# Kernel optimization log

Hardware: AMD Instinct MI355X
Metric: run time of the kernel (lower is better)

The kernel has to match this reference:

```python
import jax, jax.numpy as jnp
import numpy as np

M, N = 24, 12
H1 = (M + N) * 10 * 8        # 2880
HID = (M * M + N * N) * 10   # 7200
H2 = M * N * 4               # 1152
DOUT = M * N                 # 288
EPS = 1e-12


def setup_inputs() -> dict:
    key = jax.random.key(0)
    ks = jax.random.split(key, 16)
    s = 0.02  # weight scale
    return {
        "yt": jax.random.normal(ks[0], (N,), jnp.float32),
        "F": jax.random.normal(ks[1], (M, M), jnp.float32) * 0.1,
        "Hm": jax.random.normal(ks[2], (N, M), jnp.float32) * 0.1,
        "m1x_posterior": jax.random.normal(ks[3], (M, 1), jnp.float32),
        "m1x_prior_old": jax.random.normal(ks[4], (M, 1), jnp.float32),
        "hn": jax.random.normal(ks[5], (HID,), jnp.float32),
        "W1": jax.random.normal(ks[6], (H1, M + N), jnp.float32) * s,
        "b1": jax.random.normal(ks[7], (H1,), jnp.float32) * s,
        "Wih": jax.random.normal(ks[8], (3 * HID, H1), jnp.float32) * s,
        "Whh": jax.random.normal(ks[9], (3 * HID, HID), jnp.float32) * s,
        "bih": jax.random.normal(ks[10], (3 * HID,), jnp.float32) * s,
        "bhh": jax.random.normal(ks[11], (3 * HID,), jnp.float32) * s,
        "W2": jax.random.normal(ks[12], (H2, HID), jnp.float32) * s,
        "b2": jax.random.normal(ks[13], (H2,), jnp.float32) * s,
        "W3": jax.random.normal(ks[14], (DOUT, H2), jnp.float32) * s,
        "b3": jax.random.normal(ks[15], (DOUT,), jnp.float32) * s,
    }


def _l2_normalize(x):
    # torch F.normalize(p=2, dim=0, eps=1e-12)
    return x / jnp.maximum(jnp.linalg.norm(x), EPS)


def _gru_cell(x, h, Wih, Whh, bih, bhh):
    gi = Wih @ x + bih            # [3*HID]
    gh = Whh @ h + bhh            # [3*HID]
    gi_r, gi_z, gi_n = jnp.split(gi, 3)
    gh_r, gh_z, gh_n = jnp.split(gh, 3)
    r = jax.nn.sigmoid(gi_r + gh_r)
    z = jax.nn.sigmoid(gi_z + gh_z)
    n = jnp.tanh(gi_n + r * gh_n)
    return (1.0 - z) * n + z * h


def reference(yt, F, Hm, m1x_posterior, m1x_prior_old, hn,
              W1, b1, Wih, Whh, bih, bhh, W2, b2, W3, b3):
    # step_prior
    m1x_prior = F @ m1x_posterior        # [M,1]
    m1y = Hm @ m1x_prior                 # [N,1]
    # step_KGain_est
    dm1x = _l2_normalize((m1x_posterior - m1x_prior_old)[:, 0])  # [M]
    dm1y = _l2_normalize(yt - m1y[:, 0])                         # [N]
    kg_in = jnp.concatenate([dm1y, dm1x])                        # [M+N]
    l1 = jax.nn.relu(W1 @ kg_in + b1)                            # [H1]
    h_new = _gru_cell(l1, hn, Wih, Whh, bih, bhh)                # [HID]
    l2 = jax.nn.relu(W2 @ h_new + b2)                            # [H2]
    kg = (W3 @ l2 + b3).reshape(M, N)                            # Kalman gain
    # KNet_step update
    dy = yt[:, None] - m1y                                       # [N,1]
    m1x_post_new = m1x_prior + kg @ dy                           # [M,1]
    return m1x_post_new[:, 0]
```

## Files before the change

### kernel.cpp

```cpp
#include <hip/hip_runtime.h>
#include <math.h>

#define M_DIM 24
#define N_DIM 12
#define H1    2880
#define HID   7200
#define H2    1152
#define DOUT  288
#define KGIN  (M_DIM + N_DIM)

#define WS_PRIOR 0
#define WS_DY    96
#define WS_L1    128
#define WS_HNEW  3072
#define WS_L2    10304
#define WS_GI    11520

__device__ __forceinline__ float wave_sum(float v) {
    #pragma unroll
    for (int o = 32; o; o >>= 1) v += __shfl_xor(v, o);
    return v;
}

__global__ __launch_bounds__(256) void k_l1h(
        const float* __restrict__ yt, const float* __restrict__ F,
        const float* __restrict__ Hm, const float* __restrict__ post,
        const float* __restrict__ prior_old,
        const float* __restrict__ W1, const float* __restrict__ b1,
        float* __restrict__ ws) {
    __shared__ float s_prior[M_DIM];
    __shared__ float s_m1y[N_DIM];
    __shared__ float s_x[KGIN];
    __shared__ float s_dy[N_DIM];
    int t = threadIdx.x, lane = t & 63, w = t >> 6;

    if (t < M_DIM) {
        float acc = 0.f;
        #pragma unroll
        for (int j = 0; j < M_DIM; ++j) acc += F[t * M_DIM + j] * post[j];
        s_prior[t] = acc;
    }
    __syncthreads();
    if (t < N_DIM) {
        float acc = 0.f;
        #pragma unroll
        for (int j = 0; j < M_DIM; ++j) acc += Hm[t * M_DIM + j] * s_prior[j];
        s_m1y[t] = acc;
    }
    __syncthreads();
    if (w == 0) {
        float vx = 0.f;
        if (lane < M_DIM) vx = post[lane] - prior_old[lane];
        float nx = fmaxf(sqrtf(wave_sum(vx * vx)), 1e-12f);
        float vy = 0.f;
        if (lane < N_DIM) vy = yt[lane] - s_m1y[lane];
        float ny = fmaxf(sqrtf(wave_sum(vy * vy)), 1e-12f);
        if (lane < N_DIM) { s_x[lane] = vy / ny; s_dy[lane] = vy; }
        if (lane < M_DIM) s_x[N_DIM + lane] = vx / nx;
    }
    __syncthreads();

    if (blockIdx.x == 0) {
        if (t < M_DIM) ws[WS_PRIOR + t] = s_prior[t];
        if (t < N_DIM) ws[WS_DY + t] = s_dy[t];
    }

    int i = blockIdx.x * 4 + w;
    float acc = (lane < KGIN) ? W1[(size_t)i * KGIN + lane] * s_x[lane] : 0.f;
    acc = wave_sum(acc);
    if (lane == 0) ws[WS_L1 + i] = fmaxf(acc + b1[i], 0.f);
}

__global__ __launch_bounds__(256, 8) void k_gi(
        const float* __restrict__ Wih, const float* __restrict__ bih,
        float* __restrict__ ws) {
    int t = threadIdx.x, lane = t & 63, w = t >> 6;
    int i = blockIdx.x * 4 + w;
    const float4* x1 = (const float4*)(ws + WS_L1);
    const float4* wr = (const float4*)(Wih + (size_t)i * H1);
    const float4* wz = (const float4*)(Wih + (size_t)(i + HID) * H1);
    const float4* wn = (const float4*)(Wih + (size_t)(i + 2 * HID) * H1);
    float ar = 0.f, az = 0.f, an = 0.f;
    #pragma unroll 2
    for (int k = lane; k < H1 / 4; k += 64) {
        float4 x = x1[k];
        float4 a = wr[k], b = wz[k], c = wn[k];
        ar += a.x * x.x + a.y * x.y + a.z * x.z + a.w * x.w;
        az += b.x * x.x + b.y * x.y + b.z * x.z + b.w * x.w;
        an += c.x * x.x + c.y * x.y + c.z * x.z + c.w * x.w;
    }
    ar = wave_sum(ar); az = wave_sum(az); an = wave_sum(an);
    if (lane == 0) {
        ws[WS_GI + i]           = ar + bih[i];
        ws[WS_GI + HID + i]     = az + bih[i + HID];
        ws[WS_GI + 2 * HID + i] = an + bih[i + 2 * HID];
    }
}

__global__ __launch_bounds__(256, 8) void k_gh(
        const float* __restrict__ Whh, const float* __restrict__ bhh,
        const float* __restrict__ hn, float* __restrict__ ws) {
    int t = threadIdx.x, lane = t & 63, w = t >> 6;
    int i = blockIdx.x * 4 + w;
    const float4* xh = (const float4*)hn;
    const float4* ur = (const float4*)(Whh + (size_t)i * HID);
    const float4* uz = (const float4*)(Whh + (size_t)(i + HID) * HID);
    const float4* un = (const float4*)(Whh + (size_t)(i + 2 * HID) * HID);
    float hr = 0.f, hz = 0.f, hh = 0.f;
    #pragma unroll 2
    for (int k = lane; k < HID / 4; k += 64) {
        float4 x = xh[k];
        float4 a = ur[k], b = uz[k], c = un[k];
        hr += a.x * x.x + a.y * x.y + a.z * x.z + a.w * x.w;
        hz += b.x * x.x + b.y * x.y + b.z * x.z + b.w * x.w;
        hh += c.x * x.x + c.y * x.y + c.z * x.z + c.w * x.w;
    }
    hr = wave_sum(hr); hz = wave_sum(hz); hh = wave_sum(hh);
    if (lane == 0) {
        float gr = ws[WS_GI + i] + hr + bhh[i];
        float gz = ws[WS_GI + HID + i] + hz + bhh[i + HID];
        float r = 1.f / (1.f + expf(-gr));
        float z = 1.f / (1.f + expf(-gz));
        float n = tanhf(ws[WS_GI + 2 * HID + i] + r * (hh + bhh[i + 2 * HID]));
        ws[WS_HNEW + i] = (1.f - z) * n + z * hn[i];
    }
}

__global__ __launch_bounds__(256, 8) void k_l2(
        const float* __restrict__ W2, const float* __restrict__ b2,
        float* __restrict__ ws) {
    int t = threadIdx.x, lane = t & 63, w = t >> 6;
    int i = blockIdx.x * 4 + w;
    const float4* x4 = (const float4*)(ws + WS_HNEW);
    const float4* wr = (const float4*)(W2 + (size_t)i * HID);
    float acc = 0.f;
    #pragma unroll 2
    for (int k = lane; k < HID / 4; k += 64) {
        float4 x = x4[k];
        float4 a = wr[k];
        acc += a.x * x.x + a.y * x.y + a.z * x.z + a.w * x.w;
    }
    acc = wave_sum(acc);
    if (lane == 0) ws[WS_L2 + i] = fmaxf(acc + b2[i], 0.f);
}

__global__ __launch_bounds__(768) void k_kg_out(
        const float* __restrict__ W3, const float* __restrict__ b3,
        const float* __restrict__ ws, float* __restrict__ out) {
    __shared__ float s_kg[N_DIM];
    int m = blockIdx.x;
    int t = threadIdx.x, lane = t & 63, w = t >> 6;
    int row = m * N_DIM + w;
    const float4* wr = (const float4*)(W3 + (size_t)row * H2);
    const float4* x4 = (const float4*)(ws + WS_L2);
    float acc = 0.f;
    for (int k = lane; k < H2 / 4; k += 64) {
        float4 x = x4[k];
        float4 a = wr[k];
        acc += a.x * x.x + a.y * x.y + a.z * x.z + a.w * x.w;
    }
    acc = wave_sum(acc);
    if (lane == 0) s_kg[w] = acc + b3[row];
    __syncthreads();
    if (t == 0) {
        float a = ws[WS_PRIOR + m];
        #pragma unroll
        for (int n = 0; n < N_DIM; ++n) a += s_kg[n] * ws[WS_DY + n];
        out[m] = a;
    }
}

extern "C" void kernel_launch(void* const* d_in, const int* in_sizes, int n_in,
                              void* d_out, int out_size, void* d_ws, size_t ws_size,
                              hipStream_t stream) {
    const float* yt        = (const float*)d_in[0];
    const float* F         = (const float*)d_in[1];
    const float* Hm        = (const float*)d_in[2];
    const float* post      = (const float*)d_in[3];
    const float* prior_old = (const float*)d_in[4];
    const float* hn        = (const float*)d_in[5];
    const float* W1        = (const float*)d_in[6];
    const float* b1        = (const float*)d_in[7];
    const float* Wih       = (const float*)d_in[8];
    const float* Whh       = (const float*)d_in[9];
    const float* bih       = (const float*)d_in[10];
    const float* bhh       = (const float*)d_in[11];
    const float* W2        = (const float*)d_in[12];
    const float* b2        = (const float*)d_in[13];
    const float* W3        = (const float*)d_in[14];
    const float* b3        = (const float*)d_in[15];
    float* out = (float*)d_out;
    float* ws  = (float*)d_ws;

    k_l1h   <<<H1 / 4, 256, 0, stream>>>(yt, F, Hm, post, prior_old, W1, b1, ws);
    k_gi    <<<HID / 4, 256, 0, stream>>>(Wih, bih, ws);
    k_gh    <<<HID / 4, 256, 0, stream>>>(Whh, bhh, hn, ws);
    k_l2    <<<H2 / 4, 256, 0, stream>>>(W2, b2, ws);
    k_kg_out<<<M_DIM, 768, 0, stream>>>(W3, b3, ws, out);
}
```

Before: 184.3 us.

## Merge GRU input and hidden gate GEMVs into one launch, widen L2 GEMV

The separate Wih and Whh GEMV kernels become one launch whose first half of blocks computes the input gates and second half the hidden gates. Partial results are written to workspace, and a small new kernel applies the GRU nonlinearities. This lets the two large weight streams share a single grid instead of running back to back, at the cost of an extra launch and extra workspace traffic. The L2 GEMV now uses one 256-thread block per output row instead of one wave per row, so it launches more blocks for the 1152 rows.

```diff
diff --git a/kernel.cpp b/kernel.cpp
--- a/kernel.cpp
+++ b/kernel.cpp
@@ -9,12 +9,16 @@
 #define DOUT  288
 #define KGIN  (M_DIM + N_DIM)
 
+#define GI_BLOCKS (HID / 4)
+#define GH_BLOCKS (HID / 4)
+
 #define WS_PRIOR 0
 #define WS_DY    96
 #define WS_L1    128
 #define WS_HNEW  3072
 #define WS_L2    10304
 #define WS_GI    11520
+#define WS_GH    33152
 
 __device__ __forceinline__ float wave_sum(float v) {
     #pragma unroll
@@ -71,57 +75,66 @@
     if (lane == 0) ws[WS_L1 + i] = fmaxf(acc + b1[i], 0.f);
 }
 
-__global__ __launch_bounds__(256, 8) void k_gi(
-        const float* __restrict__ Wih, const float* __restrict__ bih,
-        float* __restrict__ ws) {
-    int t = threadIdx.x, lane = t & 63, w = t >> 6;
-    int i = blockIdx.x * 4 + w;
-    const float4* x1 = (const float4*)(ws + WS_L1);
-    const float4* wr = (const float4*)(Wih + (size_t)i * H1);
-    const float4* wz = (const float4*)(Wih + (size_t)(i + HID) * H1);
-    const float4* wn = (const float4*)(Wih + (size_t)(i + 2 * HID) * H1);
-    float ar = 0.f, az = 0.f, an = 0.f;
-    #pragma unroll 2
-    for (int k = lane; k < H1 / 4; k += 64) {
-        float4 x = x1[k];
-        float4 a = wr[k], b = wz[k], c = wn[k];
-        ar += a.x * x.x + a.y * x.y + a.z * x.z + a.w * x.w;
-        az += b.x * x.x + b.y * x.y + b.z * x.z + b.w * x.w;
-        an += c.x * x.x + c.y * x.y + c.z * x.z + c.w * x.w;
-    }
-    ar = wave_sum(ar); az = wave_sum(az); an = wave_sum(an);
-    if (lane == 0) {
-        ws[WS_GI + i]           = ar + bih[i];
-        ws[WS_GI + HID + i]     = az + bih[i + HID];
-        ws[WS_GI + 2 * HID + i] = an + bih[i + 2 * HID];
-    }
-}
-
-__global__ __launch_bounds__(256, 8) void k_gh(
-        const float* __restrict__ Whh, const float* __restrict__ bhh,
+__global__ __launch_bounds__(256, 8) void k_gates(
+        const float* __restrict__ Wih, const float* __restrict__ Whh,
+        const float* __restrict__ bih, const float* __restrict__ bhh,
         const float* __restrict__ hn, float* __restrict__ ws) {
     int t = threadIdx.x, lane = t & 63, w = t >> 6;
-    int i = blockIdx.x * 4 + w;
-    const float4* xh = (const float4*)hn;
-    const float4* ur = (const float4*)(Whh + (size_t)i * HID);
-    const float4* uz = (const float4*)(Whh + (size_t)(i + HID) * HID);
-    const float4* un = (const float4*)(Whh + (size_t)(i + 2 * HID) * HID);
-    float hr = 0.f, hz = 0.f, hh = 0.f;
-    #pragma unroll 2
-    for (int k = lane; k < HID / 4; k += 64) {
-        float4 x = xh[k];
-        float4 a = ur[k], b = uz[k], c = un[k];
-        hr += a.x * x.x + a.y * x.y + a.z * x.z + a.w * x.w;
-        hz += b.x * x.x + b.y * x.y + b.z * x.z + b.w * x.w;
-        hh += c.x * x.x + c.y * x.y + c.z * x.z + c.w * x.w;
-    }
-    hr = wave_sum(hr); hz = wave_sum(hz); hh = wave_sum(hh);
-    if (lane == 0) {
-        float gr = ws[WS_GI + i] + hr + bhh[i];
-        float gz = ws[WS_GI + HID + i] + hz + bhh[i + HID];
+    int b = blockIdx.x;
+    if (b < GI_BLOCKS) {
+        int i = b * 4 + w;
+        const float4* x1 = (const float4*)(ws + WS_L1);
+        const float4* wr = (const float4*)(Wih + (size_t)i * H1);
+        const float4* wz = (const float4*)(Wih + (size_t)(i + HID) * H1);
+        const float4* wn = (const float4*)(Wih + (size_t)(i + 2 * HID) * H1);
+        float ar = 0.f, az = 0.f, an = 0.f;
+        #pragma unroll 2
+        for (int k = lane; k < H1 / 4; k += 64) {
+            float4 x = x1[k];
+            float4 a = wr[k], bb = wz[k], c = wn[k];
+            ar += a.x * x.x + a.y * x.y + a.z * x.z + a.w * x.w;
+            az += bb.x * x.x + bb.y * x.y + bb.z * x.z + bb.w * x.w;
+            an += c.x * x.x + c.y * x.y + c.z * x.z + c.w * x.w;
+        }
+        ar = wave_sum(ar); az = wave_sum(az); an = wave_sum(an);
+        if (lane == 0) {
+            ws[WS_GI + i]           = ar + bih[i];
+            ws[WS_GI + HID + i]     = az + bih[i + HID];
+            ws[WS_GI + 2 * HID + i] = an + bih[i + 2 * HID];
+        }
+    } else {
+        int i = (b - GI_BLOCKS) * 4 + w;
+        const float4* xh = (const float4*)hn;
+        const float4* ur = (const float4*)(Whh + (size_t)i * HID);
+        const float4* uz = (const float4*)(Whh + (size_t)(i + HID) * HID);
+        const float4* un = (const float4*)(Whh + (size_t)(i + 2 * HID) * HID);
+        float hr = 0.f, hz = 0.f, hh = 0.f;
+        #pragma unroll 2
+        for (int k = lane; k < HID / 4; k += 64) {
+            float4 x = xh[k];
+            float4 a = ur[k], bb = uz[k], c = un[k];
+            hr += a.x * x.x + a.y * x.y + a.z * x.z + a.w * x.w;
+            hz += bb.x * x.x + bb.y * x.y + bb.z * x.z + bb.w * x.w;
+            hh += c.x * x.x + c.y * x.y + c.z * x.z + c.w * x.w;
+        }
+        hr = wave_sum(hr); hz = wave_sum(hz); hh = wave_sum(hh);
+        if (lane == 0) {
+            ws[WS_GH + i]           = hr + bhh[i];
+            ws[WS_GH + HID + i]     = hz + bhh[i + HID];
+            ws[WS_GH + 2 * HID + i] = hh + bhh[i + 2 * HID];
+        }
+    }
+}
+
+__global__ __launch_bounds__(256) void k_comb(const float* __restrict__ hn,
+                                              float* __restrict__ ws) {
+    int i = blockIdx.x * 256 + threadIdx.x;
+    if (i < HID) {
+        float gr = ws[WS_GI + i] + ws[WS_GH + i];
+        float gz = ws[WS_GI + HID + i] + ws[WS_GH + HID + i];
         float r = 1.f / (1.f + expf(-gr));
         float z = 1.f / (1.f + expf(-gz));
-        float n = tanhf(ws[WS_GI + 2 * HID + i] + r * (hh + bhh[i + 2 * HID]));
+        float n = tanhf(ws[WS_GI + 2 * HID + i] + r * ws[WS_GH + 2 * HID + i]);
         ws[WS_HNEW + i] = (1.f - z) * n + z * hn[i];
     }
 }
@@ -129,19 +142,23 @@
 __global__ __launch_bounds__(256, 8) void k_l2(
         const float* __restrict__ W2, const float* __restrict__ b2,
         float* __restrict__ ws) {
-    int t = threadIdx.x, lane = t & 63, w = t >> 6;
-    int i = blockIdx.x * 4 + w;
+    __shared__ float s_p[4];
+    int t = threadIdx.x, lane = t & 63, w = t >> 6;
+    int i = blockIdx.x;
     const float4* x4 = (const float4*)(ws + WS_HNEW);
     const float4* wr = (const float4*)(W2 + (size_t)i * HID);
     float acc = 0.f;
     #pragma unroll 2
-    for (int k = lane; k < HID / 4; k += 64) {
+    for (int k = t; k < HID / 4; k += 256) {
         float4 x = x4[k];
         float4 a = wr[k];
         acc += a.x * x.x + a.y * x.y + a.z * x.z + a.w * x.w;
     }
     acc = wave_sum(acc);
-    if (lane == 0) ws[WS_L2 + i] = fmaxf(acc + b2[i], 0.f);
+    if (lane == 0) s_p[w] = acc;
+    __syncthreads();
+    if (t == 0)
+        ws[WS_L2 + i] = fmaxf(s_p[0] + s_p[1] + s_p[2] + s_p[3] + b2[i], 0.f);
 }
 
 __global__ __launch_bounds__(768) void k_kg_out(
@@ -193,8 +210,8 @@
     float* ws  = (float*)d_ws;
 
     k_l1h   <<<H1 / 4, 256, 0, stream>>>(yt, F, Hm, post, prior_old, W1, b1, ws);
-    k_gi    <<<HID / 4, 256, 0, stream>>>(Wih, bih, ws);
-    k_gh    <<<HID / 4, 256, 0, stream>>>(Whh, bhh, hn, ws);
-    k_l2    <<<H2 / 4, 256, 0, stream>>>(W2, b2, ws);
+    k_gates <<<GI_BLOCKS + GH_BLOCKS, 256, 0, stream>>>(Wih, Whh, bih, bhh, hn, ws);
+    k_comb  <<<(HID + 255) / 256, 256, 0, stream>>>(hn, ws);
+    k_l2    <<<H2, 256, 0, stream>>>(W2, b2, ws);
     k_kg_out<<<M_DIM, 768, 0, stream>>>(W3, b3, ws, out);
 }
```

Result: faster. 175.8 us (-4.6%).
